# Kernel tuning notes

Hardware: AMD Instinct MI355X
Metric: run time of the kernel (lower is better)

The kernel has to match this reference:

```python
import jax, jax.numpy as jnp
import numpy as np

TWO_PI = 2.0 * np.pi


def setup_inputs() -> dict:
    key = jax.random.key(0)
    k1, k2 = jax.random.split(key)
    B, S, F, U = 16, 1024, 2048, 2048
    x = jax.random.normal(k1, (B, S, F), dtype=jnp.float32)
    # Dense(quantum_projection): weight [2F, U], bias [U]
    W = jax.random.normal(k2, (2 * F, U), dtype=jnp.float32) * (1.0 / np.sqrt(2 * F))
    b = jnp.zeros((U,), dtype=jnp.float32)
    return {"x": x, "W": W, "b": b}


def reference(x, W, b):
    # x: [B, S, F]
    qp = x * TWO_PI                                   # quantum_params
    quantum_enhanced = jnp.tanh(qp) + 0.1 * (jnp.sin(qp) * jnp.cos(qp * 0.5))
    # diag(outer(v, v)) == v**2 -- skip the O(F^2) matmul
    entanglement = quantum_enhanced * quantum_enhanced
    feats = jnp.concatenate([quantum_enhanced, entanglement], axis=-1)  # [B,S,2F]
    out = jnp.tanh(jnp.einsum('bsf,fu->bsu', feats, W) + b)             # [B,S,U]
    return out
```

## Files before the change

### kernel.cpp

```cpp
#include <hip/hip_runtime.h>
#include <hip/hip_bf16.h>
#include <math.h>


typedef __bf16 b16x8 __attribute__((ext_vector_type(8)));
typedef float f32x4 __attribute__((ext_vector_type(4)));

constexpr int Mdim = 16384;
constexpr int Fdim = 2048;
constexpr int Kdim = 4096;
constexpr int Ndim = 2048;

__device__ __forceinline__ float tanh_2pix(float x) {
  float ax = fabsf(x);
  float e = __expf(-12.566370614359172f * ax);
  float t = (1.0f - e) * __builtin_amdgcn_rcpf(1.0f + e);
  return copysignf(t, x);
}

__device__ __forceinline__ float fast_tanh(float x) {
  float ax = fabsf(x);
  float e = __expf(-2.0f * ax);
  float t = (1.0f - e) * __builtin_amdgcn_rcpf(1.0f + e);
  return copysignf(t, x);
}

struct __align__(16) B8 { __bf16 v[8]; };

__global__ void feats_kernel(const float* __restrict__ x, __bf16* __restrict__ feats) {
  int idx = blockIdx.x * blockDim.x + threadIdx.x;
  long i8 = (long)idx << 3;
  float4 xv0 = reinterpret_cast<const float4*>(x)[idx * 2];
  float4 xv1 = reinterpret_cast<const float4*>(x)[idx * 2 + 1];
  float q[8] = {xv0.x, xv0.y, xv0.z, xv0.w, xv1.x, xv1.y, xv1.z, xv1.w};
  B8 qe, en;
#pragma unroll
  for (int j = 0; j < 8; ++j) {
    float xx = q[j];
    float s = __builtin_amdgcn_sinf(xx);
    float c = __builtin_amdgcn_cosf(0.5f * xx);
    float v = tanh_2pix(xx) + 0.1f * s * c;
    qe.v[j] = (__bf16)v;
    en.v[j] = (__bf16)(v * v);
  }
  int m = (int)(i8 >> 11);
  int f = (int)(i8 & (Fdim - 1));
  size_t base = (size_t)m * Kdim + f;
  *reinterpret_cast<B8*>(feats + base) = qe;
  *reinterpret_cast<B8*>(feats + base + Fdim) = en;
}

__global__ void wtrans_kernel(const float* __restrict__ W, __bf16* __restrict__ Wt) {
  __shared__ float tile[32][33];
  int bn = blockIdx.x;
  int bk = blockIdx.y;
  int tx = threadIdx.x;
  int ty = threadIdx.y;
#pragma unroll
  for (int i = 0; i < 4; ++i) {
    int kk = bk * 32 + ty + i * 8;
    tile[ty + i * 8][tx] = W[(size_t)kk * Ndim + bn * 32 + tx];
  }
  __syncthreads();
#pragma unroll
  for (int i = 0; i < 4; ++i) {
    int nn = bn * 32 + ty + i * 8;
    Wt[(size_t)nn * Kdim + bk * 32 + tx] = (__bf16)tile[tx][ty + i * 8];
  }
}

typedef const __attribute__((address_space(1))) void* gptr1;
typedef __attribute__((address_space(3))) void* lptr3;

__device__ __forceinline__ void gld_lds16(const __bf16* g, __bf16* l) {
  __builtin_amdgcn_global_load_lds((gptr1)g, (lptr3)l, 16, 0, 0);
}

#define BARRIER()    asm volatile("s_barrier" ::: "memory")
#define WAIT_LGKM0() asm volatile("s_waitcnt lgkmcnt(0)" ::: "memory")
#define WAIT_VM(n)   asm volatile("s_waitcnt vmcnt(" #n ")" ::: "memory")

#define MFMA16(AV, BV, FB) do {                                               \
    __builtin_amdgcn_s_setprio(1);                                            \
    _Pragma("unroll")                                                         \
    for (int i_ = 0; i_ < 4; ++i_)                                            \
      _Pragma("unroll")                                                       \
      for (int j_ = 0; j_ < 4; ++j_)                                          \
        acc[(FB) + i_][j_] = __builtin_amdgcn_mfma_f32_16x16x32_bf16(         \
            AV[i_], BV[j_], acc[(FB) + i_][j_], 0, 0, 0);                     \
    __builtin_amdgcn_s_setprio(0);                                            \
  } while (0)

__global__ __launch_bounds__(512, 2) void gemm_tanh_kernel(
    const __bf16* __restrict__ A,
    const __bf16* __restrict__ Bt,
    const float* __restrict__ bias,
    float* __restrict__ out) {
  __shared__ __align__(16) __bf16 smem[65536];
  __bf16* const sA = smem;
  __bf16* const sB = smem + 32768;

  const int tid = threadIdx.x;
  const int wv = tid >> 6;
  const int lane = tid & 63;

  const int orig = blockIdx.y * 8 + blockIdx.x;
  const int wg = (orig & 7) * 64 + (orig >> 3);
  const int m0 = (wg >> 3) * 256;
  const int n0 = (wg & 7) * 256;

  const int wm = (wv >> 2) * 128;
  const int wn = (wv & 3) * 64;
  const int lr = lane & 15;
  const int lq = lane >> 4;

  const int L0 = wv * 128 + lane;
  const int L1 = L0 + 64;
  const int r0 = L0 >> 2, r1 = L1 >> 2;
  const int c0 = (L0 & 3) ^ ((r0 >> 1) & 3);
  const int c1 = (L1 & 3) ^ ((r1 >> 1) & 3);
  const __bf16* gA0 = A + (size_t)(m0 + r0) * Kdim + c0 * 8;
  const __bf16* gA1 = A + (size_t)(m0 + r1) * Kdim + c1 * 8;
  const __bf16* gB0 = Bt + (size_t)(n0 + r0) * Kdim + c0 * 8;
  const __bf16* gB1 = Bt + (size_t)(n0 + r1) * Kdim + c1 * 8;
  const int d0 = wv * 1024;
  const int d1 = d0 + 512;

  auto stageA = [&](int h) {
    __bf16* s = sA + (h & 3) * 8192;
    gld_lds16(gA0 + h * 32, s + d0);
    gld_lds16(gA1 + h * 32, s + d1);
  };
  auto stageB = [&](int h) {
    __bf16* s = sB + (h & 3) * 8192;
    gld_lds16(gB0 + h * 32, s + d0);
    gld_lds16(gB1 + h * 32, s + d1);
  };

  const int chunk = (lq ^ ((lr >> 1) & 3)) * 8;
  const int ard = (wm + lr) * 32 + chunk;
  const int brd = (wn + lr) * 32 + chunk;

  f32x4 acc[8][4];
#pragma unroll
  for (int i = 0; i < 8; ++i)
#pragma unroll
    for (int j = 0; j < 4; ++j) acc[i][j] = (f32x4){0.f, 0.f, 0.f, 0.f};

  b16x8 av0[4], av1[4], bv0[4], bv1[4];
  auto rdA = [&](b16x8 (&dst)[4], int slot, int fb) {
#pragma unroll
    for (int i = 0; i < 4; ++i)
      dst[i] = *reinterpret_cast<const b16x8*>(sA + slot * 8192 + ard + (fb + i) * 512);
  };
  auto rdB = [&](b16x8 (&dst)[4], int slot) {
#pragma unroll
    for (int i = 0; i < 4; ++i)
      dst[i] = *reinterpret_cast<const b16x8*>(sB + slot * 8192 + brd + i * 512);
  };

  float bval[4];
#pragma unroll
  for (int j = 0; j < 4; ++j) bval[j] = bias[n0 + wn + j * 16 + lr];
  WAIT_VM(0);

  stageA(0); stageB(0); stageA(1); stageB(1);
  WAIT_VM(4);
  stageA(2); stageB(2); stageB(3);
  WAIT_VM(6);
  BARRIER();
  rdA(av0, 0, 0); rdB(bv0, 0);

  for (int u = 0; u < 31; ++u) {
    const int h = u * 4;
    WAIT_LGKM0();              BARRIER(); stageA(h + 3);
    MFMA16(av0, bv0, 0);       rdA(av1, 0, 4);
    WAIT_LGKM0(); WAIT_VM(6);  BARRIER(); stageB(h + 4);
    MFMA16(av1, bv0, 4);       rdA(av0, 1, 0); rdB(bv1, 1);
    WAIT_LGKM0();              BARRIER(); stageA(h + 4);
    MFMA16(av0, bv1, 0);       rdA(av1, 1, 4);
    WAIT_LGKM0(); WAIT_VM(6);  BARRIER(); stageB(h + 5);
    MFMA16(av1, bv1, 4);       rdA(av0, 2, 0); rdB(bv0, 2);
    WAIT_LGKM0();              BARRIER(); stageA(h + 5);
    MFMA16(av0, bv0, 0);       rdA(av1, 2, 4);
    WAIT_LGKM0(); WAIT_VM(6);  BARRIER(); stageB(h + 6);
    MFMA16(av1, bv0, 4);       rdA(av0, 3, 0); rdB(bv1, 3);
    WAIT_LGKM0();              BARRIER(); stageA(h + 6);
    MFMA16(av0, bv1, 0);       rdA(av1, 3, 4);
    WAIT_LGKM0(); WAIT_VM(6);  BARRIER(); stageB(h + 7);
    MFMA16(av1, bv1, 4);       rdA(av0, 0, 0); rdB(bv0, 0);
  }

  WAIT_LGKM0();              BARRIER(); stageA(127);
  MFMA16(av0, bv0, 0);       rdA(av1, 0, 4);
  WAIT_LGKM0(); WAIT_VM(6);  BARRIER();
  MFMA16(av1, bv0, 4);       rdA(av0, 1, 0); rdB(bv1, 1);
  WAIT_LGKM0();              BARRIER();
  MFMA16(av0, bv1, 0);       rdA(av1, 1, 4);
  WAIT_LGKM0(); WAIT_VM(4);  BARRIER();
  MFMA16(av1, bv1, 4);       rdA(av0, 2, 0); rdB(bv0, 2);
  WAIT_LGKM0();              BARRIER();
  MFMA16(av0, bv0, 0);       rdA(av1, 2, 4);
  WAIT_LGKM0(); WAIT_VM(0);  BARRIER();
  MFMA16(av1, bv0, 4);       rdA(av0, 3, 0); rdB(bv1, 3);
  WAIT_LGKM0();              BARRIER();
  MFMA16(av0, bv1, 0);       rdA(av1, 3, 4);
  WAIT_LGKM0();
  MFMA16(av1, bv1, 4);

#pragma unroll
  for (int j = 0; j < 4; ++j) {
    const int gn = n0 + wn + j * 16 + lr;
#pragma unroll
    for (int i = 0; i < 8; ++i) {
      const int gm = m0 + wm + i * 16 + lq * 4;
#pragma unroll
      for (int r = 0; r < 4; ++r) {
        float v = acc[i][j][r] + bval[j];
        out[(size_t)(gm + r) * Ndim + gn] = fast_tanh(v);
      }
    }
  }
}

extern "C" void kernel_launch(void* const* d_in, const int* in_sizes, int n_in,
                              void* d_out, int out_size, void* d_ws, size_t ws_size,
                              hipStream_t stream) {
  const float* x = (const float*)d_in[0];
  const float* W = (const float*)d_in[1];
  const float* b = (const float*)d_in[2];
  float* out = (float*)d_out;

  __bf16* Wt = (__bf16*)d_ws;
  __bf16* feats = Wt + (size_t)Ndim * Kdim;

  hipLaunchKernelGGL(feats_kernel, dim3(Mdim * Fdim / 8 / 256), dim3(256), 0,
                     stream, x, feats);
  hipLaunchKernelGGL(wtrans_kernel, dim3(Ndim / 32, Kdim / 32), dim3(32, 8), 0,
                     stream, W, Wt);
  hipLaunchKernelGGL(gemm_tanh_kernel, dim3(Ndim / 256, Mdim / 256), dim3(512),
                     0, stream, feats, Wt, b, out);
}
```

Measured before the change: 487.9 us.

## Restructure GEMM main loop with merged A/B staging and interleaved LDS reads

Merges the separate A and B global-to-LDS stage calls into one combined stage per k-step. The loop now runs two k-steps per iteration with half as many barriers, and issues the LDS reads for the next fragment before the current MFMA block. It adds sched_group_barrier hints so the compiler interleaves ds_reads and VMEM loads with MFMAs. The aim is to cut barrier count and hide LDS latency behind MFMA work, at the risk of the compiler honouring the schedule hints poorly or of added register pressure.

Measured after the change: 503.1 us. 3.1% more time.

```diff
diff --git a/kernel.cpp b/kernel.cpp
--- a/kernel.cpp
+++ b/kernel.cpp
@@ -79,6 +79,7 @@
 #define BARRIER()    asm volatile("s_barrier" ::: "memory")
 #define WAIT_LGKM0() asm volatile("s_waitcnt lgkmcnt(0)" ::: "memory")
 #define WAIT_VM(n)   asm volatile("s_waitcnt vmcnt(" #n ")" ::: "memory")
+#define SGB          __builtin_amdgcn_sched_group_barrier
 
 #define MFMA16(AV, BV, FB) do {                                               \
     __builtin_amdgcn_s_setprio(1);                                            \
@@ -89,6 +90,20 @@
         acc[(FB) + i_][j_] = __builtin_amdgcn_mfma_f32_16x16x32_bf16(         \
             AV[i_], BV[j_], acc[(FB) + i_][j_], 0, 0, 0);                     \
     __builtin_amdgcn_s_setprio(0);                                            \
+  } while (0)
+
+#define ILA() do {                                                            \
+    _Pragma("unroll")                                                         \
+    for (int q_ = 0; q_ < 4; ++q_) { SGB(0x100, 1, 0); SGB(0x008, 4, 0); }    \
+  } while (0)
+#define ILB() do {                                                            \
+    SGB(0x020, 4, 0);                                                         \
+    _Pragma("unroll")                                                         \
+    for (int q_ = 0; q_ < 4; ++q_) { SGB(0x100, 2, 0); SGB(0x008, 4, 0); }    \
+  } while (0)
+#define ILB0() do {                                                           \
+    _Pragma("unroll")                                                         \
+    for (int q_ = 0; q_ < 4; ++q_) { SGB(0x100, 2, 0); SGB(0x008, 4, 0); }    \
   } while (0)
 
 __global__ __launch_bounds__(512, 2) void gemm_tanh_kernel(
@@ -126,15 +141,13 @@
   const int d0 = wv * 1024;
   const int d1 = d0 + 512;
 
-  auto stageA = [&](int h) {
-    __bf16* s = sA + (h & 3) * 8192;
-    gld_lds16(gA0 + h * 32, s + d0);
-    gld_lds16(gA1 + h * 32, s + d1);
-  };
-  auto stageB = [&](int h) {
-    __bf16* s = sB + (h & 3) * 8192;
-    gld_lds16(gB0 + h * 32, s + d0);
-    gld_lds16(gB1 + h * 32, s + d1);
+  auto stageAB = [&](int h) {
+    __bf16* a = sA + (h & 3) * 8192;
+    __bf16* b = sB + (h & 3) * 8192;
+    gld_lds16(gA0 + h * 32, a + d0);
+    gld_lds16(gA1 + h * 32, a + d1);
+    gld_lds16(gB0 + h * 32, b + d0);
+    gld_lds16(gB1 + h * 32, b + d1);
   };
 
   const int chunk = (lq ^ ((lr >> 1) & 3)) * 8;
@@ -147,7 +160,7 @@
 #pragma unroll
     for (int j = 0; j < 4; ++j) acc[i][j] = (f32x4){0.f, 0.f, 0.f, 0.f};
 
-  b16x8 av0[4], av1[4], bv0[4], bv1[4];
+  b16x8 av0[4], av1[4], bvE[4], bvO[4];
   auto rdA = [&](b16x8 (&dst)[4], int slot, int fb) {
 #pragma unroll
     for (int i = 0; i < 4; ++i)
@@ -164,49 +177,70 @@
   for (int j = 0; j < 4; ++j) bval[j] = bias[n0 + wn + j * 16 + lr];
   WAIT_VM(0);
 
-  stageA(0); stageB(0); stageA(1); stageB(1);
-  WAIT_VM(4);
-  stageA(2); stageB(2); stageB(3);
-  WAIT_VM(6);
-  BARRIER();
-  rdA(av0, 0, 0); rdB(bv0, 0);
-
-  for (int u = 0; u < 31; ++u) {
-    const int h = u * 4;
-    WAIT_LGKM0();              BARRIER(); stageA(h + 3);
-    MFMA16(av0, bv0, 0);       rdA(av1, 0, 4);
-    WAIT_LGKM0(); WAIT_VM(6);  BARRIER(); stageB(h + 4);
-    MFMA16(av1, bv0, 4);       rdA(av0, 1, 0); rdB(bv1, 1);
-    WAIT_LGKM0();              BARRIER(); stageA(h + 4);
-    MFMA16(av0, bv1, 0);       rdA(av1, 1, 4);
-    WAIT_LGKM0(); WAIT_VM(6);  BARRIER(); stageB(h + 5);
-    MFMA16(av1, bv1, 4);       rdA(av0, 2, 0); rdB(bv0, 2);
-    WAIT_LGKM0();              BARRIER(); stageA(h + 5);
-    MFMA16(av0, bv0, 0);       rdA(av1, 2, 4);
-    WAIT_LGKM0(); WAIT_VM(6);  BARRIER(); stageB(h + 6);
-    MFMA16(av1, bv0, 4);       rdA(av0, 3, 0); rdB(bv1, 3);
-    WAIT_LGKM0();              BARRIER(); stageA(h + 6);
-    MFMA16(av0, bv1, 0);       rdA(av1, 3, 4);
-    WAIT_LGKM0(); WAIT_VM(6);  BARRIER(); stageB(h + 7);
-    MFMA16(av1, bv1, 4);       rdA(av0, 0, 0); rdB(bv0, 0);
-  }
-
-  WAIT_LGKM0();              BARRIER(); stageA(127);
-  MFMA16(av0, bv0, 0);       rdA(av1, 0, 4);
-  WAIT_LGKM0(); WAIT_VM(6);  BARRIER();
-  MFMA16(av1, bv0, 4);       rdA(av0, 1, 0); rdB(bv1, 1);
-  WAIT_LGKM0();              BARRIER();
-  MFMA16(av0, bv1, 0);       rdA(av1, 1, 4);
-  WAIT_LGKM0(); WAIT_VM(4);  BARRIER();
-  MFMA16(av1, bv1, 4);       rdA(av0, 2, 0); rdB(bv0, 2);
-  WAIT_LGKM0();              BARRIER();
-  MFMA16(av0, bv0, 0);       rdA(av1, 2, 4);
-  WAIT_LGKM0(); WAIT_VM(0);  BARRIER();
-  MFMA16(av1, bv0, 4);       rdA(av0, 3, 0); rdB(bv1, 3);
-  WAIT_LGKM0();              BARRIER();
-  MFMA16(av0, bv1, 0);       rdA(av1, 3, 4);
-  WAIT_LGKM0();
-  MFMA16(av1, bv1, 4);
+  stageAB(0); stageAB(1); stageAB(2);
+  WAIT_VM(8);
+  BARRIER();
+  rdA(av0, 0, 0); rdB(bvE, 0);
+
+  for (int t = 0; t < 62; ++t) {
+    const int h = 2 * t;
+    const int s0 = h & 3, s1 = (h + 1) & 3, s2 = (h + 2) & 3;
+    WAIT_LGKM0();
+    rdA(av1, s0, 4);
+    MFMA16(av0, bvE, 0);
+    ILA();
+    WAIT_LGKM0(); WAIT_VM(4);
+    BARRIER();
+    stageAB(h + 3);
+    rdA(av0, s1, 0); rdB(bvO, s1);
+    MFMA16(av1, bvE, 4);
+    ILB();
+    WAIT_LGKM0();
+    rdA(av1, s1, 4);
+    MFMA16(av0, bvO, 0);
+    ILA();
+    WAIT_LGKM0(); WAIT_VM(4);
+    BARRIER();
+    stageAB(h + 4);
+    rdA(av0, s2, 0); rdB(bvE, s2);
+    MFMA16(av1, bvO, 4);
+    ILB();
+  }
+
+  WAIT_LGKM0();
+  rdA(av1, 0, 4);
+  MFMA16(av0, bvE, 0);
+  ILA();
+  WAIT_LGKM0(); WAIT_VM(4);
+  BARRIER();
+  stageAB(127);
+  rdA(av0, 1, 0); rdB(bvO, 1);
+  MFMA16(av1, bvE, 4);
+  ILB();
+  WAIT_LGKM0();
+  rdA(av1, 1, 4);
+  MFMA16(av0, bvO, 0);
+  ILA();
+  WAIT_LGKM0(); WAIT_VM(4);
+  BARRIER();
+  rdA(av0, 2, 0); rdB(bvE, 2);
+  MFMA16(av1, bvO, 4);
+  ILB0();
+  WAIT_LGKM0();
+  rdA(av1, 2, 4);
+  MFMA16(av0, bvE, 0);
+  ILA();
+  WAIT_LGKM0(); WAIT_VM(0);
+  BARRIER();
+  rdA(av0, 3, 0); rdB(bvO, 3);
+  MFMA16(av1, bvE, 4);
+  ILB0();
+  WAIT_LGKM0();
+  rdA(av1, 3, 4);
+  MFMA16(av0, bvO, 0);
+  ILA();
+  WAIT_LGKM0();
+  MFMA16(av1, bvO, 4);
 
 #pragma unroll
   for (int j = 0; j < 4; ++j) {
```
